# Performance work log

Measured on AMD Instinct MI355X. Metric: run time of the kernel, lower is better.

The kernel has to match this reference:

```python
import jax, jax.numpy as jnp
import numpy as np

FP8_MAX = 448.0      # max normal of float8_e4m3fn
BLOCK = 128          # TPUGEMMLinear.block_size default
INFO_THRESHOLD = 0.1
NUM_PATHS = 4


def act_quant(x, block=BLOCK):
    """Block-wise fp8 quantization along the last dim. Returns (q, scale) with
    q fp8_e4m3 of shape [..., n_blocks, block] and scale [..., n_blocks, 1]."""
    b = min(block, x.shape[-1])
    xb = x.reshape(*x.shape[:-1], x.shape[-1] // b, b)
    scale = jnp.max(jnp.abs(xb), axis=-1, keepdims=True) / FP8_MAX
    scale = jnp.maximum(scale, 1e-12)  # avoid div-by-zero
    xq = (xb / scale).astype(jnp.float8_e4m3fn)
    return xq, scale


def dequant(xq, scale, shape):
    return (xq.astype(jnp.float32) * scale).reshape(shape)


def quantize_roundtrip(x):
    xq, xs = act_quant(x)
    return dequant(xq, xs, x.shape)


def setup_inputs() -> dict:
    key = jax.random.key(0)
    k_x, k_ik, k_pk = jax.random.split(key, 3)
    N, D, F, P = 32768, 1024, 1024, NUM_PATHS
    Fp = F // P
    x = jax.random.normal(k_x, (N, D), dtype=jnp.float32)
    # lecun_normal init: std = 1/sqrt(fan_in)
    info_kernel = jax.random.normal(k_ik, (D, P), dtype=jnp.float32) / np.sqrt(D)
    info_bias = jnp.zeros((P,), dtype=jnp.float32)
    path_kernels = jax.random.normal(k_pk, (P, D, Fp), dtype=jnp.float32) / np.sqrt(D)
    path_biases = jnp.zeros((P, Fp), dtype=jnp.float32)
    return {"x": x, "info_kernel": info_kernel, "info_bias": info_bias,
            "path_kernels": path_kernels, "path_biases": path_biases}


def reference(x, info_kernel, info_bias, path_kernels, path_biases):
    N, D = x.shape
    P = info_kernel.shape[-1]
    # fp8 quantize/dequant round trips (simulated fp8 GEMM: dequant then matmul)
    xd = quantize_roundtrip(x)                      # [N, D]
    ikd = quantize_roundtrip(info_kernel)           # [D, P]
    pkd = quantize_roundtrip(path_kernels)          # [P, D, Fp]
    # info-gain gating
    info_net = xd @ ikd + info_bias                 # [N, P]
    info_gains = jax.nn.sigmoid(info_net)
    cumul_info = info_gains                         # prev_info defaults to zeros
    # training=True: soft path weights
    path_weights = jax.nn.sigmoid((cumul_info - INFO_THRESHOLD) * 10.0)  # [N, P]
    # per-path projections (batched GEMM) + per-path chunk weighting
    path_out = jnp.einsum('nd,pdf->npf', xd, pkd) + path_biases          # [N, P, Fp]
    out = (path_out * path_weights[:, :, None]).reshape(N, -1)           # [N, F]
    return out, cumul_info
```

## Files before the change

### kernel.cpp

```cpp
#include <hip/hip_runtime.h>
#include <hip/hip_bf16.h>
#include <stdint.h>


typedef float v2f __attribute__((ext_vector_type(2)));
typedef float f32x4 __attribute__((ext_vector_type(4)));
typedef __bf16 bf16x8 __attribute__((ext_vector_type(8)));
typedef unsigned short us4 __attribute__((ext_vector_type(4)));

__device__ __forceinline__ unsigned short f2bf(float f) {
  unsigned u = __builtin_bit_cast(unsigned, f);
  u += 0x7fffu + ((u >> 16) & 1u);
  return (unsigned short)(u >> 16);
}

__device__ __forceinline__ v2f fp8_rt2s(float a, float b, float sa, float sb) {
  int q = __builtin_amdgcn_cvt_pk_fp8_f32(a / sa, b / sb, 0, false);
  v2f r = __builtin_amdgcn_cvt_pk_f32_fp8(q, false);
  r.x *= sa;
  r.y *= sb;
  return r;
}

__device__ __forceinline__ v2f fp8_rt2i(float a, float b, float s, float inv) {
  int q = __builtin_amdgcn_cvt_pk_fp8_f32(a * inv, b * inv, 0, false);
  v2f r = __builtin_amdgcn_cvt_pk_f32_fp8(q, false);
  r.x *= s;
  r.y *= s;
  return r;
}

__device__ __forceinline__ unsigned pk_bf16(float lo, float hi) {
  unsigned r;
  asm("v_cvt_pk_bf16_f32 %0, %1, %2" : "=v"(r) : "v"(lo), "v"(hi));
  return r;
}

__device__ __forceinline__ void g2l16(const void* g, void* l) {
  __builtin_amdgcn_global_load_lds(
      (const __attribute__((address_space(1))) unsigned int*)g,
      (__attribute__((address_space(3))) unsigned int*)l,
      16, 0, 0);
}

__global__ __launch_bounds__(256) void k_quant_info(
    const float* __restrict__ x, const float* __restrict__ ik,
    const float* __restrict__ ib, unsigned short* __restrict__ xd,
    float* __restrict__ pw, float* __restrict__ cumul, int N) {
  const int tid = threadIdx.x;
  const int lane = tid & 63, wv = tid >> 6;
  const int gw = blockIdx.x * 4 + wv;
  const int nw = gridDim.x * 4;

  f32x4 kv[16];
#pragma unroll
  for (int q = 0; q < 16; ++q) {
    const int d = lane * 16 + q;
    f32x4 v = ((const f32x4*)ik)[d];
    float m = fmaxf(fmaxf(fabsf(v.x), fabsf(v.y)), fmaxf(fabsf(v.z), fabsf(v.w)));
    float s = fmaxf(m * (1.0f / 448.0f), 1e-12f);
    v2f lo = fp8_rt2s(v.x, v.y, s, s);
    v2f hi = fp8_rt2s(v.z, v.w, s, s);
    f32x4 dq; dq.x = lo.x; dq.y = lo.y; dq.z = hi.x; dq.w = hi.y;
    kv[q] = dq;
  }
  const f32x4 ibv = *(const f32x4*)ib;

  for (int row = gw; row < N; row += nw) {
    const f32x4* xr = (const f32x4*)(x + (size_t)row * 1024) + lane * 4;
    f32x4 v0 = xr[0], v1 = xr[1], v2 = xr[2], v3 = xr[3];

    float m = fmaxf(fmaxf(fabsf(v0.x), fabsf(v0.y)), fmaxf(fabsf(v0.z), fabsf(v0.w)));
    m = fmaxf(m, fmaxf(fmaxf(fabsf(v1.x), fabsf(v1.y)), fmaxf(fabsf(v1.z), fabsf(v1.w))));
    m = fmaxf(m, fmaxf(fmaxf(fabsf(v2.x), fabsf(v2.y)), fmaxf(fabsf(v2.z), fabsf(v2.w))));
    m = fmaxf(m, fmaxf(fmaxf(fabsf(v3.x), fabsf(v3.y)), fmaxf(fabsf(v3.z), fabsf(v3.w))));
    m = fmaxf(m, __shfl_xor(m, 1, 64));
    m = fmaxf(m, __shfl_xor(m, 2, 64));
    m = fmaxf(m, __shfl_xor(m, 4, 64));
    const float s = fmaxf(m * (1.0f / 448.0f), 1e-12f);
    const float inv = __builtin_amdgcn_rcpf(s);

    float p0 = 0.f, p1 = 0.f, p2 = 0.f, p3 = 0.f;
    unsigned w[8];
#define QPAIR(J, A, B)                                            \
    {                                                             \
      v2f r = fp8_rt2i((A), (B), s, inv);                         \
      f32x4 ka = kv[2 * (J)], kb = kv[2 * (J) + 1];               \
      p0 += r.x * ka.x + r.y * kb.x;                              \
      p1 += r.x * ka.y + r.y * kb.y;                              \
      p2 += r.x * ka.z + r.y * kb.z;                              \
      p3 += r.x * ka.w + r.y * kb.w;                              \
      w[J] = pk_bf16(r.x, r.y);                                   \
    }
    QPAIR(0, v0.x, v0.y) QPAIR(1, v0.z, v0.w)
    QPAIR(2, v1.x, v1.y) QPAIR(3, v1.z, v1.w)
    QPAIR(4, v2.x, v2.y) QPAIR(5, v2.z, v2.w)
    QPAIR(6, v3.x, v3.y) QPAIR(7, v3.z, v3.w)
#undef QPAIR

    uint4* dst = (uint4*)(xd + (size_t)row * 1024 + lane * 16);
    uint4 o0; o0.x = w[0]; o0.y = w[1]; o0.z = w[2]; o0.w = w[3];
    uint4 o1; o1.x = w[4]; o1.y = w[5]; o1.z = w[6]; o1.w = w[7];
    dst[0] = o0; dst[1] = o1;

#pragma unroll
    for (int off = 1; off <= 32; off <<= 1) {
      p0 += __shfl_xor(p0, off, 64);
      p1 += __shfl_xor(p1, off, 64);
      p2 += __shfl_xor(p2, off, 64);
      p3 += __shfl_xor(p3, off, 64);
    }

    const int pl = lane & 3;
    float pv = p0;
    pv = (pl == 1) ? p1 : pv;
    pv = (pl == 2) ? p2 : pv;
    pv = (pl == 3) ? p3 : pv;
    float bb = ibv.x;
    bb = (pl == 1) ? ibv.y : bb;
    bb = (pl == 2) ? ibv.z : bb;
    bb = (pl == 3) ? ibv.w : bb;
    float g = __builtin_amdgcn_rcpf(1.f + __expf(-(pv + bb)));
    float wgt = __builtin_amdgcn_rcpf(1.f + __expf(-((g - 0.1f) * 10.f)));
    if (lane < 4) {
      cumul[(size_t)row * 4 + pl] = g;
      pw[(size_t)row * 4 + pl] = wgt;
    }
  }
}

__global__ __launch_bounds__(256) void k_quant_pk(
    const float* __restrict__ pk, unsigned short* __restrict__ bt) {
  __shared__ float s_x[32 * 256];
  __shared__ float s_s[32 * 2];
  const int tid = threadIdx.x;
  const int lane = tid & 63, wv = tid >> 6;
  const int p = blockIdx.x >> 5;
  const int d0 = (blockIdx.x & 31) * 32;

  const f32x4* src = (const f32x4*)(pk + ((size_t)p * 1024 + d0) * 256);
  f32x4* dst = (f32x4*)s_x;
#pragma unroll
  for (int i = 0; i < 8; ++i) {
    f32x4 v = src[tid + i * 256];
    dst[tid + i * 256] = v;
    float m = fmaxf(fmaxf(fabsf(v.x), fabsf(v.y)), fmaxf(fabsf(v.z), fabsf(v.w)));
#pragma unroll
    for (int off = 1; off <= 16; off <<= 1)
      m = fmaxf(m, __shfl_xor(m, off, 64));
    if ((lane & 31) == 0)
      s_s[(wv + 4 * i) * 2 + (lane >> 5)] = fmaxf(m * (1.0f / 448.0f), 1e-12f);
  }
  __syncthreads();

  const int f = tid;
  uint4 hv[4];
  unsigned* hw = (unsigned*)hv;
#pragma unroll
  for (int d = 0; d < 32; d += 2) {
    float v0 = s_x[d * 256 + f];
    float sa = s_s[d * 2 + (f >> 7)];
    float v1 = s_x[(d + 1) * 256 + f];
    float sb = s_s[(d + 1) * 2 + (f >> 7)];
    v2f r = fp8_rt2s(v0, v1, sa, sb);
    hw[d >> 1] = (unsigned)f2bf(r.x) | ((unsigned)f2bf(r.y) << 16);
  }
  unsigned short* orow = bt + (size_t)(p * 256 + f) * 1024 + d0;
  uint4* ov = (uint4*)orow;
#pragma unroll
  for (int i = 0; i < 4; ++i) ov[i] = hv[i];
}

__global__ __launch_bounds__(256) void k_gemm(
    const unsigned short* __restrict__ xd, const unsigned short* __restrict__ bt,
    const float* __restrict__ pb, const float* __restrict__ pw,
    float* __restrict__ out, int N) {
  __shared__ __align__(16) unsigned short As[128 * 64];
  __shared__ __align__(16) unsigned short Bs[128 * 64];
  const int tid = threadIdx.x;
  const int lane = tid & 63, wv = tid >> 6;
  const int nwg = gridDim.x, cpx = nwg >> 3;
  const int bx = (blockIdx.x & 7) * cpx + (blockIdx.x >> 3);
  const int tm = bx >> 3, tn = bx & 7;
  const int m0 = tm * 128, f0 = tn * 128;
  const int wr = wv >> 1, wc = wv & 1;

  f32x4 acc[4][4] = {};
  const int frow = lane & 15;
  const int fk = (lane >> 4) * 8;

  for (int k0 = 0; k0 < 1024; k0 += 64) {
    __syncthreads();
#pragma unroll
    for (int i = 0; i < 4; ++i) {
      const int cbase = (wv * 4 + i) * 64;
      const int chunk = cbase + lane;
      const int r = chunk >> 3, c8 = chunk & 7;
      g2l16(xd + (size_t)(m0 + r) * 1024 + k0 + c8 * 8, (char*)As + cbase * 16);
      g2l16(bt + (size_t)(f0 + r) * 1024 + k0 + c8 * 8, (char*)Bs + cbase * 16);
    }
    __syncthreads();
#pragma unroll
    for (int kk = 0; kk < 64; kk += 32) {
      bf16x8 af[4], bfr[4];
#pragma unroll
      for (int mi = 0; mi < 4; ++mi)
        af[mi] = *(const bf16x8*)&As[(wr * 64 + mi * 16 + frow) * 64 + kk + fk];
#pragma unroll
      for (int ni = 0; ni < 4; ++ni)
        bfr[ni] = *(const bf16x8*)&Bs[(wc * 64 + ni * 16 + frow) * 64 + kk + fk];
#pragma unroll
      for (int mi = 0; mi < 4; ++mi)
#pragma unroll
        for (int ni = 0; ni < 4; ++ni)
          acc[mi][ni] = __builtin_amdgcn_mfma_f32_16x16x32_bf16(
              af[mi], bfr[ni], acc[mi][ni], 0, 0, 0);
    }
  }

  const int r0 = m0 + wr * 64 + (lane >> 4) * 4;
  const int c0 = f0 + wc * 64 + frow;
#pragma unroll
  for (int ni = 0; ni < 4; ++ni) {
    const int c = c0 + ni * 16;
    const float bias = pb[c];
    const int p = c >> 8;
#pragma unroll
    for (int mi = 0; mi < 4; ++mi) {
#pragma unroll
      for (int r = 0; r < 4; ++r) {
        const int row = r0 + mi * 16 + r;
        out[(size_t)row * 1024 + c] = (acc[mi][ni][r] + bias) * pw[row * 4 + p];
      }
    }
  }
}

extern "C" void kernel_launch(void* const* d_in, const int* in_sizes, int n_in,
                              void* d_out, int out_size, void* d_ws, size_t ws_size,
                              hipStream_t stream) {
  const float* x  = (const float*)d_in[0];
  const float* ik = (const float*)d_in[1];
  const float* ib = (const float*)d_in[2];
  const float* pk = (const float*)d_in[3];
  const float* pb = (const float*)d_in[4];
  const int N = in_sizes[0] / 1024;

  float* out = (float*)d_out;
  float* cumul = out + (size_t)N * 1024;

  char* ws = (char*)d_ws;
  unsigned short* xd = (unsigned short*)ws;
  unsigned short* bt = (unsigned short*)(ws + (size_t)N * 1024 * 2);
  float* pw = (float*)(ws + (size_t)N * 1024 * 2 + (size_t)1024 * 1024 * 2);

  hipLaunchKernelGGL(k_quant_info, dim3(2048), dim3(256), 0, stream,
                     x, ik, ib, xd, pw, cumul, N);
  hipLaunchKernelGGL(k_quant_pk, dim3(128), dim3(256), 0, stream, pk, bt);
  hipLaunchKernelGGL(k_gemm, dim3((N / 128) * 8), dim3(256), 0, stream,
                     xd, bt, pb, pw, out, N);
}
```

Baseline: 359.6 us.

## Rewrite GEMM as 256x256 double-buffered, swizzled, ping-pong MFMA kernel

The GEMM tile grows from 128x128 with 4 waves to 256x256 with 8 waves. LDS is now double-buffered so the next K slice loads while the current one computes. LDS columns are XOR-swizzled to avoid bank conflicts, and barriers plus s_setprio alternate load and MFMA phases across waves. The aim is to hide global-load latency and raise MFMA utilisation, at the cost of 128KB of LDS, higher register pressure and fewer workgroups (512), which may limit occupancy and leave the wave quantisation across CUs uneven.

```diff
diff --git a/kernel.cpp b/kernel.cpp
--- a/kernel.cpp
+++ b/kernel.cpp
@@ -171,69 +171,142 @@
   for (int i = 0; i < 4; ++i) ov[i] = hv[i];
 }
 
-__global__ __launch_bounds__(256) void k_gemm(
+__global__ __launch_bounds__(512, 2) void k_gemm(
     const unsigned short* __restrict__ xd, const unsigned short* __restrict__ bt,
     const float* __restrict__ pb, const float* __restrict__ pw,
     float* __restrict__ out, int N) {
-  __shared__ __align__(16) unsigned short As[128 * 64];
-  __shared__ __align__(16) unsigned short Bs[128 * 64];
+  __shared__ __align__(16) unsigned short Asm[2][256 * 64];
+  __shared__ __align__(16) unsigned short Bsm[2][256 * 64];
   const int tid = threadIdx.x;
   const int lane = tid & 63, wv = tid >> 6;
   const int nwg = gridDim.x, cpx = nwg >> 3;
   const int bx = (blockIdx.x & 7) * cpx + (blockIdx.x >> 3);
-  const int tm = bx >> 3, tn = bx & 7;
-  const int m0 = tm * 128, f0 = tn * 128;
-  const int wr = wv >> 1, wc = wv & 1;
-
-  f32x4 acc[4][4] = {};
+  const int tm = bx >> 2, tn = bx & 3;
+  const int m0 = tm * 256, f0 = tn * 256;
+  const int wr = wv >> 2, wc = wv & 3;
   const int frow = lane & 15;
-  const int fk = (lane >> 4) * 8;
-
-  for (int k0 = 0; k0 < 1024; k0 += 64) {
-    __syncthreads();
-#pragma unroll
-    for (int i = 0; i < 4; ++i) {
-      const int cbase = (wv * 4 + i) * 64;
-      const int chunk = cbase + lane;
-      const int r = chunk >> 3, c8 = chunk & 7;
-      g2l16(xd + (size_t)(m0 + r) * 1024 + k0 + c8 * 8, (char*)As + cbase * 16);
-      g2l16(bt + (size_t)(f0 + r) * 1024 + k0 + c8 * 8, (char*)Bs + cbase * 16);
-    }
-    __syncthreads();
-#pragma unroll
-    for (int kk = 0; kk < 64; kk += 32) {
-      bf16x8 af[4], bfr[4];
-#pragma unroll
-      for (int mi = 0; mi < 4; ++mi)
-        af[mi] = *(const bf16x8*)&As[(wr * 64 + mi * 16 + frow) * 64 + kk + fk];
-#pragma unroll
-      for (int ni = 0; ni < 4; ++ni)
-        bfr[ni] = *(const bf16x8*)&Bs[(wc * 64 + ni * 16 + frow) * 64 + kk + fk];
-#pragma unroll
-      for (int mi = 0; mi < 4; ++mi)
-#pragma unroll
-        for (int ni = 0; ni < 4; ++ni)
-          acc[mi][ni] = __builtin_amdgcn_mfma_f32_16x16x32_bf16(
-              af[mi], bfr[ni], acc[mi][ni], 0, 0, 0);
-    }
-  }
-
-  const int r0 = m0 + wr * 64 + (lane >> 4) * 4;
+  const int fkc = lane >> 4;
+  const int rsw = frow & 7;
+
+  const int srow = (lane >> 3);
+  const int scol = lane & 7;
+
+  f32x4 acc[8][4] = {};
+
+#define STAGE(dA, dB, ks)                                                  \
+  {                                                                        \
+    _Pragma("unroll")                                                      \
+    for (int i = 0; i < 4; ++i) {                                          \
+      const int cb = i * 8 + wv;                                           \
+      const int r = cb * 8 + srow;                                         \
+      const int cc = scol ^ (r & 7);  \
+      g2l16(xd + (size_t)(m0 + r) * 1024 + (ks) + cc * 8,                  \
+            (char*)(dA) + cb * 1024);                                      \
+      g2l16(bt + (size_t)(f0 + r) * 1024 + (ks) + cc * 8,                  \
+            (char*)(dB) + cb * 1024);                                      \
+    }                                                                      \
+  }
+
+#define LDA4(dst, buf, msub, k32)                                          \
+  {                                                                        \
+    const int cc = ((((k32) >> 3) + fkc) ^ rsw) * 8;                       \
+    _Pragma("unroll")                                                      \
+    for (int fi = 0; fi < 4; ++fi) {                                       \
+      const int rr = wr * 128 + (msub) * 64 + fi * 16 + frow;              \
+      dst[fi] = *(const bf16x8*)&(buf)[rr * 64 + cc];                      \
+    }                                                                      \
+  }
+
+#define LDB4(dst, buf, k32)                                                \
+  {                                                                        \
+    const int cc = ((((k32) >> 3) + fkc) ^ rsw) * 8;                       \
+    _Pragma("unroll")                                                      \
+    for (int fi = 0; fi < 4; ++fi) {                                       \
+      const int rr = wc * 64 + fi * 16 + frow;                             \
+      dst[fi] = *(const bf16x8*)&(buf)[rr * 64 + cc];                      \
+    }                                                                      \
+  }
+
+#define MFMA16(mb, a, b)                                                   \
+  {                                                                        \
+    _Pragma("unroll")                                                      \
+    for (int ni = 0; ni < 4; ++ni)                                         \
+      _Pragma("unroll")                                                    \
+      for (int mi = 0; mi < 4; ++mi)                                       \
+        acc[(mb) * 4 + mi][ni] = __builtin_amdgcn_mfma_f32_16x16x32_bf16(  \
+            a[mi], b[ni], acc[(mb) * 4 + mi][ni], 0, 0, 0);                \
+  }
+
+  STAGE(Asm[0], Bsm[0], 0)
+  STAGE(Asm[1], Bsm[1], 64)
+  asm volatile("s_waitcnt vmcnt(8)" ::: "memory");
+  __builtin_amdgcn_sched_barrier(0);
+  __builtin_amdgcn_s_barrier();
+
+  for (int t = 0; t < 16; ++t) {
+    const int p = t & 1;
+    const unsigned short* Ab = Asm[p];
+    const unsigned short* Bb = Bsm[p];
+    bf16x8 a[4], b[4];
+
+    LDB4(b, Bb, 0)
+    LDA4(a, Ab, 0, 0)
+    if (t >= 1 && t < 15) {
+      STAGE(Asm[p ^ 1], Bsm[p ^ 1], (t + 1) * 64)
+    }
+    __builtin_amdgcn_s_barrier();
+    __builtin_amdgcn_s_setprio(1);
+    MFMA16(0, a, b)
+    __builtin_amdgcn_s_setprio(0);
+    __builtin_amdgcn_s_barrier();
+
+    LDA4(a, Ab, 1, 0)
+    __builtin_amdgcn_s_barrier();
+    __builtin_amdgcn_s_setprio(1);
+    MFMA16(1, a, b)
+    __builtin_amdgcn_s_setprio(0);
+    __builtin_amdgcn_s_barrier();
+
+    LDB4(b, Bb, 32)
+    LDA4(a, Ab, 0, 32)
+    __builtin_amdgcn_s_barrier();
+    __builtin_amdgcn_s_setprio(1);
+    MFMA16(0, a, b)
+    __builtin_amdgcn_s_setprio(0);
+    __builtin_amdgcn_s_barrier();
+
+    LDA4(a, Ab, 1, 32)
+    __builtin_amdgcn_s_barrier();
+    __builtin_amdgcn_s_setprio(1);
+    MFMA16(1, a, b)
+    __builtin_amdgcn_s_setprio(0);
+    if (t < 15) {
+      asm volatile("s_waitcnt vmcnt(0)" ::: "memory");
+      __builtin_amdgcn_sched_barrier(0);
+    }
+    __builtin_amdgcn_s_barrier();
+  }
+
+  const int r0 = m0 + wr * 128 + (lane >> 4) * 4;
   const int c0 = f0 + wc * 64 + frow;
 #pragma unroll
   for (int ni = 0; ni < 4; ++ni) {
     const int c = c0 + ni * 16;
     const float bias = pb[c];
-    const int p = c >> 8;
-#pragma unroll
-    for (int mi = 0; mi < 4; ++mi) {
+    const int pp = c >> 8;
+#pragma unroll
+    for (int mi = 0; mi < 8; ++mi) {
 #pragma unroll
       for (int r = 0; r < 4; ++r) {
         const int row = r0 + mi * 16 + r;
-        out[(size_t)row * 1024 + c] = (acc[mi][ni][r] + bias) * pw[row * 4 + p];
+        out[(size_t)row * 1024 + c] = (acc[mi][ni][r] + bias) * pw[row * 4 + pp];
       }
     }
   }
+#undef STAGE
+#undef LDA4
+#undef LDB4
+#undef MFMA16
 }
 
 extern "C" void kernel_launch(void* const* d_in, const int* in_sizes, int n_in,
@@ -257,6 +330,6 @@
   hipLaunchKernelGGL(k_quant_info, dim3(2048), dim3(256), 0, stream,
                      x, ik, ib, xd, pw, cumul, N);
   hipLaunchKernelGGL(k_quant_pk, dim3(128), dim3(256), 0, stream, pk, bt);
-  hipLaunchKernelGGL(k_gemm, dim3((N / 128) * 8), dim3(256), 0, stream,
+  hipLaunchKernelGGL(k_gemm, dim3((N / 256) * 4), dim3(512), 0, stream,
                      xd, bt, pb, pw, out, N);
 }
```

New measurement: 364.6 us. Within noise of the previous version (+1.4%).
